# Kernel optimization log

Hardware: AMD Instinct MI355X
Metric: run time of the kernel (lower is better)

## Reference

```python
import jax, jax.numpy as jnp
import numpy as np

B, L, D, H = 2, 2048, 1024, 16
DK = D // H  # 64

def setup_inputs() -> dict:
    key = jax.random.key(0)
    ks = jax.random.split(key, 9)
    s = 1.0 / np.sqrt(D)
    return {
        "X":  jax.random.normal(ks[0], (B, L, D), dtype=jnp.float32),
        "WQ": jax.random.uniform(ks[1], (D, H * DK), jnp.float32, -s, s),
        "bQ": jax.random.uniform(ks[2], (H * DK,), jnp.float32, -s, s),
        "WK": jax.random.uniform(ks[3], (D, H * DK), jnp.float32, -s, s),
        "bK": jax.random.uniform(ks[4], (H * DK,), jnp.float32, -s, s),
        "WV": jax.random.uniform(ks[5], (D, H * DK), jnp.float32, -s, s),
        "bV": jax.random.uniform(ks[6], (H * DK,), jnp.float32, -s, s),
        "WO": jax.random.uniform(ks[7], (H * DK, D), jnp.float32, -s, s),
        "bO": jax.random.uniform(ks[8], (D,), jnp.float32, -s, s),
    }

def reference(X, WQ, bQ, WK, bK, WV, bV, WO, bO):
    b, l, d = X.shape
    # Linear projections, split into heads: (b, h, l, d_k)
    Q = (X @ WQ + bQ).reshape(b, l, H, DK).transpose(0, 2, 1, 3)
    K = (X @ WK + bK).reshape(b, l, H, DK).transpose(0, 2, 1, 3)
    V = (X @ WV + bV).reshape(b, l, H, DK).transpose(0, 2, 1, 3)
    # Full L x L scores (mask=None path: all-ones mask is a no-op)
    scores = jnp.einsum('bhqd,bhkd->bhqk', Q, K) / jnp.sqrt(jnp.float32(DK))
    A = jax.nn.softmax(scores, axis=-1)
    out = jnp.einsum('bhqk,bhkd->bhqd', A, V)          # (b, h, l, d_v)
    out = out.transpose(0, 2, 1, 3).reshape(b, l, H * DK)
    return out @ WO + bO
```

## Files before the change

kernel.cpp:

```cpp
#include <hip/hip_runtime.h>
#include <stdint.h>

#define BB 2
#define HH 16
#define LL 2048
#define DD 1024

typedef __bf16 b16x8 __attribute__((ext_vector_type(8)));
typedef float f32x4 __attribute__((ext_vector_type(4)));
typedef int i32x4 __attribute__((ext_vector_type(4)));

__device__ __forceinline__ short f2bf(float f) {
  unsigned u = __builtin_bit_cast(unsigned, f);
  return (short)((u + 0x7fffu + ((u >> 16) & 1u)) >> 16);
}

__device__ __forceinline__ short bfc(float f) {
  return __builtin_bit_cast(short, static_cast<__bf16>(f));
}

__device__ __forceinline__ int cvtpk(float lo, float hi) {
  int r;
  asm("v_cvt_pk_bf16_f32 %0, %1, %2" : "=v"(r) : "v"(lo), "v"(hi));
  return r;
}

__device__ __forceinline__ void gl_lds16(const void* gp, void* lp) {
  __builtin_amdgcn_global_load_lds(
      (const __attribute__((address_space(1))) void*)gp,
      (__attribute__((address_space(3))) void*)lp, 16, 0, 0);
}

__global__ __launch_bounds__(256) void prep(const float* __restrict__ X,
                                            short* __restrict__ Xb,
                                            const float* __restrict__ W0,
                                            const float* __restrict__ W1,
                                            const float* __restrict__ W2,
                                            const float* __restrict__ W3,
                                            short* __restrict__ Wt) {
  if (blockIdx.z == 4) {
    int base = (blockIdx.y * 32 + blockIdx.x) * 1024 + threadIdx.x;
#pragma unroll
    for (int k = 0; k < 4; ++k) {
      int i = base + k * 256;
      float4 v = ((const float4*)X)[i];
      short4 o;
      o.x = f2bf(v.x); o.y = f2bf(v.y); o.z = f2bf(v.z); o.w = f2bf(v.w);
      ((short4*)Xb)[i] = o;
    }
    return;
  }
  __shared__ float t[32][33];
  const float* W = blockIdx.z == 0 ? W0 : blockIdx.z == 1 ? W1
                 : blockIdx.z == 2 ? W2 : W3;
  short* dst = Wt + (size_t)blockIdx.z * DD * DD;
  int tx = threadIdx.x & 31, ty0 = threadIdx.x >> 5;
  int nb = blockIdx.x * 32, kb = blockIdx.y * 32;
#pragma unroll
  for (int i = 0; i < 4; ++i)
    t[ty0 + i * 8][tx] = W[(size_t)(kb + ty0 + i * 8) * DD + nb + tx];
  __syncthreads();
#pragma unroll
  for (int i = 0; i < 4; ++i)
    dst[(size_t)(nb + ty0 + i * 8) * DD + kb + tx] = f2bf(t[tx][ty0 + i * 8]);
}

__global__ __launch_bounds__(256) void qkv_gemm(const short* __restrict__ Xb,
                                                const short* __restrict__ Wall,
                                                const float* __restrict__ bQ,
                                                const float* __restrict__ bK,
                                                const float* __restrict__ bV,
                                                short* __restrict__ Qo,
                                                short* __restrict__ Ko,
                                                short* __restrict__ Vto) {
  __shared__ __align__(16) short As[128 * 32];
  __shared__ __align__(16) short Bs[128 * 32];

  const int tid = threadIdx.x;
  const int lane = tid & 63;
  const int wid = tid >> 6;
  const int orig = blockIdx.x + 24 * blockIdx.y;
  const int nid = (orig & 7) * 96 + (orig >> 3);
  const int m0 = (nid & 31) * 128;
  const int ng = (nid >> 5) * 128;
  const int sel = ng >> 10;
  const int n0 = ng & 1023;
  const short* W = Wall + (size_t)sel * DD * DD;

  const int wrow = wid >> 1, wcol = wid & 1;
  const int lrow = lane & 15;
  const int hi = lane >> 4;
  const int sl8 = (hi ^ ((lrow >> 1) & 3)) * 8;
  const int srow = lane >> 2;
  const int scol = ((lane & 3) ^ ((lane >> 3) & 3)) * 8;

  f32x4 z4 = {0.f, 0.f, 0.f, 0.f};
  f32x4 acc[4][4];
#pragma unroll
  for (int i = 0; i < 4; ++i)
#pragma unroll
    for (int j = 0; j < 4; ++j) acc[i][j] = z4;

  for (int kt = 0; kt < DD; kt += 32) {
#pragma unroll
    for (int i = 0; i < 2; ++i) {
      int c = wid * 2 + i;
      gl_lds16(Xb + (size_t)(m0 + c * 16 + srow) * DD + kt + scol, As + c * 512);
      gl_lds16(W + (size_t)(n0 + c * 16 + srow) * DD + kt + scol, Bs + c * 512);
    }
    __syncthreads();
    b16x8 a[4], b[4];
#pragma unroll
    for (int i = 0; i < 4; ++i)
      a[i] = *(const b16x8*)(As + (wrow * 64 + i * 16 + lrow) * 32 + sl8);
#pragma unroll
    for (int j = 0; j < 4; ++j)
      b[j] = *(const b16x8*)(Bs + (wcol * 64 + j * 16 + lrow) * 32 + sl8);
#pragma unroll
    for (int i = 0; i < 4; ++i)
#pragma unroll
      for (int j = 0; j < 4; ++j)
        acc[i][j] = __builtin_amdgcn_mfma_f32_16x16x32_bf16(a[i], b[j], acc[i][j], 0, 0, 0);
    __syncthreads();
  }

  const float* bias = sel == 0 ? bQ : sel == 1 ? bK : bV;
  float bv[4];
#pragma unroll
  for (int j = 0; j < 4; ++j) bv[j] = bias[n0 + wcol * 64 + j * 16 + lrow];

  const int rbase = hi * 4;
  if (sel == 2) {
#pragma unroll
    for (int i = 0; i < 4; ++i) {
      int gm = m0 + wrow * 64 + i * 16 + rbase;
      int bb = gm >> 11, lb = gm & 2047;
      int x = lb & 63;
      int kf = x >> 4;
      int lbp = (lb & ~63) | ((kf >> 1) << 5) | (((x >> 2) & 3) << 3) | ((kf & 1) << 2);
#pragma unroll
      for (int j = 0; j < 4; ++j) {
        int gn = n0 + wcol * 64 + j * 16 + lrow;
        int h = gn >> 6, dk = gn & 63;
        short4 pk;
        pk.x = bfc(acc[i][j][0] + bv[j]);
        pk.y = bfc(acc[i][j][1] + bv[j]);
        pk.z = bfc(acc[i][j][2] + bv[j]);
        pk.w = bfc(acc[i][j][3] + bv[j]);
        *(short4*)(Vto + ((size_t)((bb * HH + h) * 64 + dk)) * LL + lbp) = pk;
      }
    }
  } else {
    short* dst = sel == 0 ? Qo : Ko;
    float sc = sel == 0 ? 0.18033688011112042f : 1.0f;
#pragma unroll
    for (int i = 0; i < 4; ++i) {
      int gm = m0 + wrow * 64 + i * 16 + rbase;
#pragma unroll
      for (int j = 0; j < 4; ++j) {
        int gn = n0 + wcol * 64 + j * 16 + lrow;
        int h = gn >> 6, dk = gn & 63;
#pragma unroll
        for (int r = 0; r < 4; ++r) {
          int m = gm + r;
          int bb = m >> 11, lq = m & 2047;
          dst[((size_t)(bb * HH + h) * LL + lq) * 64 + dk] =
              bfc((acc[i][j][r] + bv[j]) * sc);
        }
      }
    }
  }
}

__global__ __launch_bounds__(256, 2) void attn(const short* __restrict__ Qg,
                                               const short* __restrict__ Kg,
                                               const short* __restrict__ Vt,
                                               short* __restrict__ Og) {
  __shared__ __align__(16) short Ks[3][64 * 64];
  __shared__ __align__(16) short Vs[3][64 * 64];

  const int tid = threadIdx.x;
  const int lane = tid & 63;
  const int wid = tid >> 6;

  const int orig = blockIdx.x + 16 * blockIdx.y;
  const int nid = (orig & 7) * 64 + (orig >> 3);
  const int bh = nid >> 4;
  const int q0 = (nid & 15) * 128 + wid * 32;

  const short* Qb = Qg + (size_t)bh * LL * 64;
  const short* Kb = Kg + (size_t)bh * LL * 64;
  const short* Vb = Vt + (size_t)bh * 64 * LL;

  const int lrow = lane & 15;
  const int hi = lane >> 4;
  const int hi8 = hi * 8;
  const int hi16b = hi * 16;
  const int r8 = lane >> 3;
  const int c8 = lane & 7;
  const int swz8 = (c8 ^ r8) * 8;

  b16x8 qf[2][2];
#pragma unroll
  for (int f = 0; f < 2; ++f)
#pragma unroll
    for (int ks = 0; ks < 2; ++ks)
      qf[f][ks] = *(const b16x8*)(Qb + (size_t)(q0 + f * 16 + lrow) * 64 + ks * 32 + hi8);

  f32x4 z4 = {0.f, 0.f, 0.f, 0.f};
  f32x4 accO[2][4];
  float nm[2], l_i[2];
#pragma unroll
  for (int f = 0; f < 2; ++f) {
#pragma unroll
    for (int d = 0; d < 4; ++d) accO[f][d] = z4;
    nm[f] = 0.f; l_i[f] = 0.f;
  }

  int offs[4][2];
#pragma unroll
  for (int a = 0; a < 4; ++a) {
    int row = a * 16 + lrow;
    int sw = (row & 7) << 4;
#pragma unroll
    for (int ks = 0; ks < 2; ++ks)
      offs[a][ks] = row * 128 + ((ks * 64 + hi16b) ^ sw);
  }

  auto stage = [&](int kt_, int buf_) {
#pragma unroll
    for (int i = 0; i < 2; ++i) {
      int c = wid * 2 + i;
      gl_lds16(Kb + (size_t)(kt_ * 64 + c * 8 + r8) * 64 + swz8, &Ks[buf_][c * 512]);
      gl_lds16(Vb + (size_t)(c * 8 + r8) * LL + kt_ * 64 + swz8, &Vs[buf_][c * 512]);
    }
  };

  stage(0, 0);
  stage(1, 1);
  asm volatile("s_waitcnt vmcnt(4)" ::: "memory");
  __builtin_amdgcn_s_barrier();

  int cur = 0;
  for (int kt = 0; kt < LL / 64; ++kt) {
    if (kt + 2 < LL / 64) {
      int pb = cur + 2;
      if (pb >= 3) pb -= 3;
      stage(kt + 2, pb);
    }

    const char* ksb = (const char*)&Ks[cur][0];
    const char* vsb = (const char*)&Vs[cur][0];

    f32x4 sacc[2][4];
#pragma unroll
    for (int f = 0; f < 2; ++f) {
      f32x4 nm4 = {nm[f], nm[f], nm[f], nm[f]};
#pragma unroll
      for (int kf = 0; kf < 4; ++kf) sacc[f][kf] = nm4;
    }

    __builtin_amdgcn_s_setprio(1);
#pragma unroll
    for (int kf = 0; kf < 4; ++kf) {
#pragma unroll
      for (int ks = 0; ks < 2; ++ks) {
        b16x8 kfr = *(const b16x8*)(ksb + offs[kf][ks]);
#pragma unroll
        for (int f = 0; f < 2; ++f)
          sacc[f][kf] =
              __builtin_amdgcn_mfma_f32_16x16x32_bf16(kfr, qf[f][ks], sacc[f][kf], 0, 0, 0);
      }
    }
    __builtin_amdgcn_s_setprio(0);

    float lm[2];
#pragma unroll
    for (int f = 0; f < 2; ++f) {
      float mx = fmaxf(fmaxf(sacc[f][0][0], sacc[f][0][1]),
                       fmaxf(sacc[f][0][2], sacc[f][0][3]));
#pragma unroll
      for (int kf = 1; kf < 4; ++kf)
        mx = fmaxf(mx, fmaxf(fmaxf(sacc[f][kf][0], sacc[f][kf][1]),
                             fmaxf(sacc[f][kf][2], sacc[f][kf][3])));
      lm[f] = mx;
    }
    float w = fmaxf(lm[0], lm[1]);

    if (!__all(w <= 8.0f)) {
#pragma unroll
      for (int f = 0; f < 2; ++f) {
        float mx = lm[f];
        mx = fmaxf(mx, __shfl_xor(mx, 16));
        mx = fmaxf(mx, __shfl_xor(mx, 32));
        float d = fmaxf(mx, 0.f);
        float corr = __builtin_amdgcn_exp2f(-d);
        l_i[f] *= corr;
        nm[f] -= d;
#pragma unroll
        for (int db = 0; db < 4; ++db) accO[f][db] *= corr;
#pragma unroll
        for (int kf = 0; kf < 4; ++kf) sacc[f][kf] -= d;
      }
    }

    b16x8 pfr[2][2];
#pragma unroll
    for (int f = 0; f < 2; ++f) {
      float ps = 0.f;
#pragma unroll
      for (int c = 0; c < 2; ++c) {
        float e0 = __builtin_amdgcn_exp2f(sacc[f][2 * c][0]);
        float e1 = __builtin_amdgcn_exp2f(sacc[f][2 * c][1]);
        float e2 = __builtin_amdgcn_exp2f(sacc[f][2 * c][2]);
        float e3 = __builtin_amdgcn_exp2f(sacc[f][2 * c][3]);
        float e4 = __builtin_amdgcn_exp2f(sacc[f][2 * c + 1][0]);
        float e5 = __builtin_amdgcn_exp2f(sacc[f][2 * c + 1][1]);
        float e6 = __builtin_amdgcn_exp2f(sacc[f][2 * c + 1][2]);
        float e7 = __builtin_amdgcn_exp2f(sacc[f][2 * c + 1][3]);
        ps += ((e0 + e1) + (e2 + e3)) + ((e4 + e5) + (e6 + e7));
        i32x4 pt;
        pt[0] = cvtpk(e0, e1);
        pt[1] = cvtpk(e2, e3);
        pt[2] = cvtpk(e4, e5);
        pt[3] = cvtpk(e6, e7);
        pfr[f][c] = __builtin_bit_cast(b16x8, pt);
      }
      l_i[f] += ps;
    }

    b16x8 vfr[4][2];
#pragma unroll
    for (int db = 0; db < 4; ++db) {
#pragma unroll
      for (int ks = 0; ks < 2; ++ks)
        vfr[db][ks] = *(const b16x8*)(vsb + offs[db][ks]);
    }

    __builtin_amdgcn_s_setprio(1);
#pragma unroll
    for (int f = 0; f < 2; ++f) {
#pragma unroll
      for (int db = 0; db < 4; ++db) {
        accO[f][db] = __builtin_amdgcn_mfma_f32_16x16x32_bf16(vfr[db][0], pfr[f][0],
                                                              accO[f][db], 0, 0, 0);
        accO[f][db] = __builtin_amdgcn_mfma_f32_16x16x32_bf16(vfr[db][1], pfr[f][1],
                                                              accO[f][db], 0, 0, 0);
      }
    }
    __builtin_amdgcn_s_setprio(0);

    if (kt + 2 < LL / 64) {
      asm volatile("s_waitcnt vmcnt(4)" ::: "memory");
      __builtin_amdgcn_s_barrier();
    } else if (kt + 1 < LL / 64) {
      asm volatile("s_waitcnt vmcnt(0)" ::: "memory");
      __builtin_amdgcn_s_barrier();
    }
    cur = cur + 1 >= 3 ? 0 : cur + 1;
  }

  const int bb = bh >> 4, h = bh & 15;
#pragma unroll
  for (int f = 0; f < 2; ++f) {
    float l = l_i[f];
    l += __shfl_xor(l, 16);
    l += __shfl_xor(l, 32);
    float rl = 1.0f / l;
    int q = q0 + f * 16 + lrow;
#pragma unroll
    for (int db = 0; db < 4; ++db) {
      short4 pk;
      pk.x = bfc(accO[f][db][0] * rl);
      pk.y = bfc(accO[f][db][1] * rl);
      pk.z = bfc(accO[f][db][2] * rl);
      pk.w = bfc(accO[f][db][3] * rl);
      *(short4*)(Og + (size_t)(bb * LL + q) * DD + h * 64 + db * 16 + hi * 4) = pk;
    }
  }
}

__global__ __launch_bounds__(256) void out_gemm(const short* __restrict__ Ab,
                                                const short* __restrict__ Wt,
                                                const float* __restrict__ bO,
                                                float* __restrict__ Out) {
  __shared__ __align__(16) short As[64 * 32];
  __shared__ __align__(16) short Bs[128 * 32];

  const int tid = threadIdx.x;
  const int lane = tid & 63;
  const int wid = tid >> 6;
  const int orig = blockIdx.x + 8 * blockIdx.y;
  const int nid = (orig & 7) * 64 + (orig >> 3);
  const int n0 = (nid >> 6) * 128;
  const int m0 = (nid & 63) * 64;

  const int wrow = wid >> 1, wcol = wid & 1;
  const int lrow = lane & 15;
  const int hi = lane >> 4;
  const int sl8 = (hi ^ ((lrow >> 1) & 3)) * 8;
  const int srow = lane >> 2;
  const int scol = ((lane & 3) ^ ((lane >> 3) & 3)) * 8;

  f32x4 z4 = {0.f, 0.f, 0.f, 0.f};
  f32x4 acc[2][4];
#pragma unroll
  for (int i = 0; i < 2; ++i)
#pragma unroll
    for (int j = 0; j < 4; ++j) acc[i][j] = z4;

  for (int kt = 0; kt < DD; kt += 32) {
    gl_lds16(Ab + (size_t)(m0 + wid * 16 + srow) * DD + kt + scol, As + wid * 512);
#pragma unroll
    for (int i = 0; i < 2; ++i) {
      int c = wid * 2 + i;
      gl_lds16(Wt + (size_t)(n0 + c * 16 + srow) * DD + kt + scol, Bs + c * 512);
    }
    __syncthreads();
    b16x8 a[2], b[4];
#pragma unroll
    for (int i = 0; i < 2; ++i)
      a[i] = *(const b16x8*)(As + (wrow * 32 + i * 16 + lrow) * 32 + sl8);
#pragma unroll
    for (int j = 0; j < 4; ++j)
      b[j] = *(const b16x8*)(Bs + (wcol * 64 + j * 16 + lrow) * 32 + sl8);
#pragma unroll
    for (int i = 0; i < 2; ++i)
#pragma unroll
      for (int j = 0; j < 4; ++j)
        acc[i][j] = __builtin_amdgcn_mfma_f32_16x16x32_bf16(a[i], b[j], acc[i][j], 0, 0, 0);
    __syncthreads();
  }

  float bv[4];
#pragma unroll
  for (int j = 0; j < 4; ++j) bv[j] = bO[n0 + wcol * 64 + j * 16 + lrow];

  const int rbase = hi * 4;
#pragma unroll
  for (int i = 0; i < 2; ++i) {
    int gm = m0 + wrow * 32 + i * 16 + rbase;
#pragma unroll
    for (int j = 0; j < 4; ++j) {
      int gn = n0 + wcol * 64 + j * 16 + lrow;
#pragma unroll
      for (int r = 0; r < 4; ++r)
        Out[(size_t)(gm + r) * DD + gn] = acc[i][j][r] + bv[j];
    }
  }
}

extern "C" void kernel_launch(void* const* d_in, const int* in_sizes, int n_in,
                              void* d_out, int out_size, void* d_ws, size_t ws_size,
                              hipStream_t stream) {
  const float* X = (const float*)d_in[0];
  const float* WQ = (const float*)d_in[1];
  const float* bQ = (const float*)d_in[2];
  const float* WK = (const float*)d_in[3];
  const float* bK = (const float*)d_in[4];
  const float* WV = (const float*)d_in[5];
  const float* bV = (const float*)d_in[6];
  const float* WO = (const float*)d_in[7];
  const float* bO = (const float*)d_in[8];
  float* Out = (float*)d_out;

  if (ws_size < (size_t)24 * 1024 * 1024 * 2) return;
  short* ws = (short*)d_ws;
  short* Xb = ws;
  short* Wt = Xb + (size_t)4096 * 1024;
  short* Qb = Wt + (size_t)4 * 1024 * 1024;
  short* Kb = Qb + (size_t)4096 * 1024;
  short* Vtb = Kb + (size_t)4096 * 1024;
  short* At = Vtb + (size_t)4096 * 1024;

  hipLaunchKernelGGL(prep, dim3(32, 32, 5), dim3(256), 0, stream, X, Xb, WQ, WK, WV, WO, Wt);
  hipLaunchKernelGGL(qkv_gemm, dim3(24, 32), dim3(256), 0, stream, Xb, Wt, bQ, bK, bV,
                     Qb, Kb, Vtb);
  hipLaunchKernelGGL(attn, dim3(16, 32), dim3(256), 0, stream, Qb, Kb, Vtb, At);
  hipLaunchKernelGGL(out_gemm, dim3(8, 64), dim3(256), 0, stream, At,
                     Wt + (size_t)3 * 1024 * 1024, bO, Out);
}
```

Measured before the change: 105.7 us.

## Process 128-key tiles per iteration with double-buffered K/V staging

The attention loop now handles 128 keys per iteration instead of 64 and drops from a three-stage to a two-stage LDS ring. This halves the number of barriers, online-softmax max checks and loop overheads, and gives more MFMA work between syncs. In exchange it keeps more score registers live (sacc doubles) and prefetches only one tile ahead with a full vmcnt(0) wait, which may reduce latency hiding and occupancy.

```diff
diff --git a/kernel.cpp b/kernel.cpp
--- a/kernel.cpp
+++ b/kernel.cpp
@@ -176,8 +176,8 @@
                                                const short* __restrict__ Kg,
                                                const short* __restrict__ Vt,
                                                short* __restrict__ Og) {
-  __shared__ __align__(16) short Ks[3][64 * 64];
-  __shared__ __align__(16) short Vs[3][64 * 64];
+  __shared__ __align__(16) short Ks[2][128 * 64];
+  __shared__ __align__(16) short Vs[2][2][64 * 64];
 
   const int tid = threadIdx.x;
   const int lane = tid & 63;
@@ -217,9 +217,9 @@
     nm[f] = 0.f; l_i[f] = 0.f;
   }
 
-  int offs[4][2];
-#pragma unroll
-  for (int a = 0; a < 4; ++a) {
+  int offs[8][2];
+#pragma unroll
+  for (int a = 0; a < 8; ++a) {
     int row = a * 16 + lrow;
     int sw = (row & 7) << 4;
 #pragma unroll
@@ -229,40 +229,41 @@
 
   auto stage = [&](int kt_, int buf_) {
 #pragma unroll
-    for (int i = 0; i < 2; ++i) {
-      int c = wid * 2 + i;
-      gl_lds16(Kb + (size_t)(kt_ * 64 + c * 8 + r8) * 64 + swz8, &Ks[buf_][c * 512]);
-      gl_lds16(Vb + (size_t)(c * 8 + r8) * LL + kt_ * 64 + swz8, &Vs[buf_][c * 512]);
-    }
+    for (int i = 0; i < 4; ++i) {
+      int c = wid * 4 + i;
+      gl_lds16(Kb + (size_t)(kt_ * 128 + c * 8 + r8) * 64 + swz8, &Ks[buf_][c * 512]);
+    }
+#pragma unroll
+    for (int s = 0; s < 2; ++s)
+#pragma unroll
+      for (int i = 0; i < 2; ++i) {
+        int c = wid * 2 + i;
+        gl_lds16(Vb + (size_t)(c * 8 + r8) * LL + kt_ * 128 + s * 64 + swz8,
+                 &Vs[buf_][s][c * 512]);
+      }
   };
 
   stage(0, 0);
-  stage(1, 1);
-  asm volatile("s_waitcnt vmcnt(4)" ::: "memory");
+  asm volatile("s_waitcnt vmcnt(0)" ::: "memory");
   __builtin_amdgcn_s_barrier();
 
-  int cur = 0;
-  for (int kt = 0; kt < LL / 64; ++kt) {
-    if (kt + 2 < LL / 64) {
-      int pb = cur + 2;
-      if (pb >= 3) pb -= 3;
-      stage(kt + 2, pb);
-    }
-
-    const char* ksb = (const char*)&Ks[cur][0];
-    const char* vsb = (const char*)&Vs[cur][0];
-
-    f32x4 sacc[2][4];
+  int buf = 0;
+  for (int kt = 0; kt < LL / 128; ++kt) {
+    if (kt + 1 < LL / 128) stage(kt + 1, buf ^ 1);
+
+    const char* ksb = (const char*)&Ks[buf][0];
+
+    f32x4 sacc[2][8];
 #pragma unroll
     for (int f = 0; f < 2; ++f) {
       f32x4 nm4 = {nm[f], nm[f], nm[f], nm[f]};
 #pragma unroll
-      for (int kf = 0; kf < 4; ++kf) sacc[f][kf] = nm4;
+      for (int kf = 0; kf < 8; ++kf) sacc[f][kf] = nm4;
     }
 
     __builtin_amdgcn_s_setprio(1);
 #pragma unroll
-    for (int kf = 0; kf < 4; ++kf) {
+    for (int kf = 0; kf < 8; ++kf) {
 #pragma unroll
       for (int ks = 0; ks < 2; ++ks) {
         b16x8 kfr = *(const b16x8*)(ksb + offs[kf][ks]);
@@ -280,7 +281,7 @@
       float mx = fmaxf(fmaxf(sacc[f][0][0], sacc[f][0][1]),
                        fmaxf(sacc[f][0][2], sacc[f][0][3]));
 #pragma unroll
-      for (int kf = 1; kf < 4; ++kf)
+      for (int kf = 1; kf < 8; ++kf)
         mx = fmaxf(mx, fmaxf(fmaxf(sacc[f][kf][0], sacc[f][kf][1]),
                              fmaxf(sacc[f][kf][2], sacc[f][kf][3])));
       lm[f] = mx;
@@ -300,16 +301,16 @@
 #pragma unroll
         for (int db = 0; db < 4; ++db) accO[f][db] *= corr;
 #pragma unroll
-        for (int kf = 0; kf < 4; ++kf) sacc[f][kf] -= d;
-      }
-    }
-
-    b16x8 pfr[2][2];
+        for (int kf = 0; kf < 8; ++kf) sacc[f][kf] -= d;
+      }
+    }
+
+    b16x8 pfr[2][4];
 #pragma unroll
     for (int f = 0; f < 2; ++f) {
       float ps = 0.f;
 #pragma unroll
-      for (int c = 0; c < 2; ++c) {
+      for (int c = 0; c < 4; ++c) {
         float e0 = __builtin_amdgcn_exp2f(sacc[f][2 * c][0]);
         float e1 = __builtin_amdgcn_exp2f(sacc[f][2 * c][1]);
         float e2 = __builtin_amdgcn_exp2f(sacc[f][2 * c][2]);
@@ -329,35 +330,29 @@
       l_i[f] += ps;
     }
 
-    b16x8 vfr[4][2];
-#pragma unroll
-    for (int db = 0; db < 4; ++db) {
-#pragma unroll
-      for (int ks = 0; ks < 2; ++ks)
-        vfr[db][ks] = *(const b16x8*)(vsb + offs[db][ks]);
-    }
+    b16x8 vfr[4][4];
+#pragma unroll
+    for (int db = 0; db < 4; ++db)
+#pragma unroll
+      for (int sl = 0; sl < 4; ++sl) {
+        const char* vsb = (const char*)&Vs[buf][sl >> 1][0];
+        vfr[db][sl] = *(const b16x8*)(vsb + offs[db][sl & 1]);
+      }
 
     __builtin_amdgcn_s_setprio(1);
 #pragma unroll
-    for (int f = 0; f < 2; ++f) {
-#pragma unroll
-      for (int db = 0; db < 4; ++db) {
-        accO[f][db] = __builtin_amdgcn_mfma_f32_16x16x32_bf16(vfr[db][0], pfr[f][0],
-                                                              accO[f][db], 0, 0, 0);
-        accO[f][db] = __builtin_amdgcn_mfma_f32_16x16x32_bf16(vfr[db][1], pfr[f][1],
-                                                              accO[f][db], 0, 0, 0);
-      }
-    }
+    for (int f = 0; f < 2; ++f)
+#pragma unroll
+      for (int db = 0; db < 4; ++db)
+#pragma unroll
+        for (int sl = 0; sl < 4; ++sl)
+          accO[f][db] = __builtin_amdgcn_mfma_f32_16x16x32_bf16(vfr[db][sl], pfr[f][sl],
+                                                                accO[f][db], 0, 0, 0);
     __builtin_amdgcn_s_setprio(0);
 
-    if (kt + 2 < LL / 64) {
-      asm volatile("s_waitcnt vmcnt(4)" ::: "memory");
-      __builtin_amdgcn_s_barrier();
-    } else if (kt + 1 < LL / 64) {
-      asm volatile("s_waitcnt vmcnt(0)" ::: "memory");
-      __builtin_amdgcn_s_barrier();
-    }
-    cur = cur + 1 >= 3 ? 0 : cur + 1;
+    asm volatile("s_waitcnt vmcnt(0)" ::: "memory");
+    __builtin_amdgcn_s_barrier();
+    buf ^= 1;
   }
 
   const int bb = bh >> 4, h = bh & 15;
```

After: 104.1 us (median of 2 runs). No clear change (-1.5%).
